# Optimization experiments

Hardware: AMD Instinct MI355X
Metric: run time of the kernel (lower is better)

Reference implementation:

```python
import jax, jax.numpy as jnp
import numpy as np
import math

PAD_IDX = 1
BOS_IDX = 2
B, S, T = 32, 128, 64
E, H, L, V = 256, 512, 2, 32000


def _lstm_cell(gates, c):
    # torch gate order: i, f, g, o
    i, f, g, o = jnp.split(gates, 4, axis=-1)
    c_new = jax.nn.sigmoid(f) * c + jax.nn.sigmoid(i) * jnp.tanh(g)
    h_new = jax.nn.sigmoid(o) * jnp.tanh(c_new)
    return h_new, c_new


def _run_lstm_layer(x_tbi, Wih, Whh, b, h0, c0):
    def step(carry, x_t):
        h, c = carry
        h2, c2 = _lstm_cell(x_t @ Wih + h @ Whh + b, c)
        return (h2, c2), h2
    (hT, cT), ys = jax.lax.scan(step, (h0, c0), x_tbi)
    return ys, hT, cT


def setup_inputs() -> dict:
    key = jax.random.key(0)
    ks = iter(jax.random.split(key, 40))
    def w(shape, s=0.05):
        return jax.random.normal(next(ks), shape, jnp.float32) * s
    inp = {
        'src_tokens': jax.random.randint(next(ks), (B, S), 0, V, dtype=jnp.int32),
        'tgt_tokens': jax.random.randint(next(ks), (B, T), 0, V, dtype=jnp.int32),
        'src_emb': w((V, E), 0.02),
        'tgt_emb': w((V, E), 0.02),
        'enc_Wih0': w((E, 4 * H)), 'enc_Whh0': w((H, 4 * H)), 'enc_b0': jnp.zeros((4 * H,), jnp.float32),
        'enc_Wih1': w((H, 4 * H)), 'enc_Whh1': w((H, 4 * H)), 'enc_b1': jnp.zeros((4 * H,), jnp.float32),
        'dec_Wih0': w((E + H, 4 * H)), 'dec_Whh0': w((H, 4 * H)), 'dec_b0': jnp.zeros((4 * H,), jnp.float32),
        'dec_Wih1': w((H, 4 * H)), 'dec_Whh1': w((H, 4 * H)), 'dec_b1': jnp.zeros((4 * H,), jnp.float32),
        'attn_W': w((2 * H, H)), 'attn_b': jnp.zeros((H,), jnp.float32),
        'v_w': w((H,)),
        'coal_w': w((L, 1), 0.5), 'coal_b': jnp.zeros((1,), jnp.float32),
        'out_W': w((2 * H + E, V)), 'out_b': jnp.zeros((V,), jnp.float32),
    }
    return inp


def reference(src_tokens, tgt_tokens, src_emb, tgt_emb,
              enc_Wih0, enc_Whh0, enc_b0, enc_Wih1, enc_Whh1, enc_b1,
              dec_Wih0, dec_Whh0, dec_b0, dec_Wih1, dec_Whh1, dec_b1,
              attn_W, attn_b, v_w, coal_w, coal_b, out_W, out_b):
    Bq = src_tokens.shape[0]
    sqrtE_src = np.float32(math.sqrt(src_emb.shape[1]))
    sqrtE_tgt = np.float32(math.sqrt(tgt_emb.shape[1]))

    # ---- Encoder (2-layer LSTM, batch_first; dropout=0 eval) ----
    x = (src_emb[src_tokens] * sqrtE_src).transpose(1, 0, 2)  # (S,B,E)
    z = jnp.zeros((Bq, H), jnp.float32)
    ys0, hA, cA = _run_lstm_layer(x, enc_Wih0, enc_Whh0, enc_b0, z, z)
    ys1, hB, cB = _run_lstm_layer(ys0, enc_Wih1, enc_Whh1, enc_b1, z, z)
    enc_out = ys1.transpose(1, 0, 2)          # (B,S,H)
    hidden = jnp.stack([hA, hB])              # (L,B,H)
    cell = jnp.stack([cA, cB])

    mask = src_tokens != PAD_IDX              # (B,S)
    Wq, We = attn_W[:H], attn_W[H:]
    enc_proj = enc_out @ We                   # (B,S,H) loop-invariant part of attn linear

    def dec_step(carry, tok):
        h, c = carry                          # (L,B,H) each
        emb = jax.nn.relu(tgt_emb[tok] * sqrtE_tgt)          # (B,E)
        # faithful raw reshape (L,B,H) -> (B,H,L), coalesce layers
        q = jax.nn.relu(h.reshape(Bq, H, L) @ coal_w + coal_b)[..., 0]  # (B,H)
        e = jnp.tanh(enc_proj + (q @ Wq + attn_b)[:, None, :])          # (B,S,H)
        score = e @ v_w                                                 # (B,S)
        score = jnp.where(mask, score, np.float32(-1e10))
        a = jax.nn.softmax(score, axis=1)
        wctx = jnp.einsum('bs,bsh->bh', a, enc_out)                     # (B,H)
        xin = jnp.concatenate([emb, wctx], axis=-1)                     # (B,E+H)
        h0n, c0n = _lstm_cell(xin @ dec_Wih0 + h[0] @ dec_Whh0 + dec_b0, c[0])
        h1n, c1n = _lstm_cell(h0n @ dec_Wih1 + h[1] @ dec_Whh1 + dec_b1, c[1])
        logits = jnp.concatenate([h1n, wctx, emb], axis=-1) @ out_W + out_b  # (B,V)
        return (jnp.stack([h0n, h1n]), jnp.stack([c0n, c1n])), logits

    (hF, cF), outs = jax.lax.scan(dec_step, (hidden, cell), tgt_tokens[:, :-1].T)
    first = jnp.full((Bq, 1, out_b.shape[0]), np.float32(BOS_IDX))  # decoder_outputs[:,0]=BOS_IDX
    dec_outputs = jnp.concatenate([first, outs.transpose(1, 0, 2)], axis=1)  # (B,T,V)
    return dec_outputs, hF, cF
```

## Files before the change

### kernel.cpp

```cpp
#include <hip/hip_runtime.h>
#include <hip/hip_bf16.h>

typedef __bf16 bf16x8 __attribute__((ext_vector_type(8)));
typedef float f32x4 __attribute__((ext_vector_type(4)));
typedef unsigned long long u64;

#define DEV static __device__ __forceinline__

constexpr int Bq = 32, Sq = 128, Tq = 64, Eq = 256, Hq = 512, Vq = 32000;
constexpr int G4 = 2048;
constexpr int TD = 63;
constexpr int KOUT = 1280;
constexpr float SQRTE = 16.0f;

DEV float sigf(float x) { return 1.0f / (1.0f + __expf(-x)); }
DEV float tanh_fast(float x) {
    float ax = fabsf(x);
    float t = __expf(-2.f * ax);
    float r = (1.f - t) / (1.f + t);
    return x < 0.f ? -r : r;
}
DEV float tanh_c(float x) {
    float xc = fminf(fmaxf(x, -15.f), 15.f);
    float t = __expf(2.f * xc);
    return (t - 1.f) / (t + 1.f);
}

DEV u64 ldc(const u64* p) {
    return __hip_atomic_load(p, __ATOMIC_RELAXED, __HIP_MEMORY_SCOPE_AGENT);
}
DEV unsigned ldc32(const unsigned* p) {
    return __hip_atomic_load(p, __ATOMIC_RELAXED, __HIP_MEMORY_SCOPE_AGENT);
}
DEV void stc(u64* p, u64 v) {
    __hip_atomic_store(p, v, __ATOMIC_RELAXED, __HIP_MEMORY_SCOPE_AGENT);
}
DEV void stc32(unsigned* p, unsigned v) {
    __hip_atomic_store(p, v, __ATOMIC_RELAXED, __HIP_MEMORY_SCOPE_AGENT);
}
DEV unsigned short bfbits(float f) {
    __bf16 h = (__bf16)f;
    return __builtin_bit_cast(unsigned short, h);
}
DEV float bf2f(unsigned short u) {
    __bf16 h = __builtin_bit_cast(__bf16, u);
    return (float)h;
}
DEV u64 pack4bf(float a, float b, float c, float d) {
    return (u64)bfbits(a) | ((u64)bfbits(b) << 16) |
           ((u64)bfbits(c) << 32) | ((u64)bfbits(d) << 48);
}
DEV u64 pack2f(float a, float b) {
    return (u64)__float_as_uint(a) | ((u64)__float_as_uint(b) << 32);
}

template<bool C> DEV u64 ld64(const u64* p) { return C ? ldc(p) : *p; }
template<bool C> DEV void st64(u64* p, u64 v) { if (C) stc(p, v); else *p = v; }

DEV void gbar(unsigned* flags, int nblk, unsigned epoch) {
    __syncthreads();
    if (threadIdx.x < 64) {
        if (threadIdx.x == 0) {
            asm volatile("s_waitcnt vmcnt(0)" ::: "memory");
            stc32(flags + blockIdx.x * 32, epoch);
        }
        int lane = threadIdx.x;
        for (;;) {
            unsigned v0 = (lane < nblk) ? ldc32(flags + lane * 32) : epoch;
            if (__all((int)(v0 >= epoch))) break;
            __builtin_amdgcn_s_sleep(1);
        }
    }
    __syncthreads();
}

__global__ __launch_bounds__(256) void k_embed_src(const int* __restrict__ tok,
                                                   const float* __restrict__ emb,
                                                   __hip_bfloat16* __restrict__ x)
{
    int idx = blockIdx.x * 256 + threadIdx.x;
    int e = idx & (Eq - 1);
    int r = idx >> 8;
    int b = r & 31, t = r >> 5;
    x[idx] = __float2bfloat16(emb[(size_t)tok[b * Sq + t] * Eq + e] * SQRTE);
}

__global__ __launch_bounds__(256) void k_embed_tgt(const int* __restrict__ tok,
                                                   const float* __restrict__ emb,
                                                   __hip_bfloat16* __restrict__ embt,
                                                   __hip_bfloat16* __restrict__ Xout)
{
    int idx = blockIdx.x * 256 + threadIdx.x;
    int e = idx & (Eq - 1);
    int r = idx >> 8;
    int b = r & 31, t = r >> 5;
    float v = fmaxf(0.f, emb[(size_t)tok[b * Tq + t] * Eq + e] * SQRTE);
    embt[idx] = __float2bfloat16(v);
    Xout[(size_t)r * KOUT + 1024 + e] = __float2bfloat16(v);
}

__global__ __launch_bounds__(256) void k_transpose_bf16(const float* __restrict__ W,
                                                        __hip_bfloat16* __restrict__ Wt,
                                                        int K, int N)
{
    __shared__ float tile[32][33];
    int nb = blockIdx.x * 32, kb = blockIdx.y * 32;
    int c = threadIdx.x & 31, r4 = threadIdx.x >> 5;
    for (int i = 0; i < 32; i += 8)
        tile[r4 + i][c] = W[(size_t)(kb + r4 + i) * N + nb + c];
    __syncthreads();
    for (int i = 0; i < 32; i += 8) {
        int rr = r4 + i;
        Wt[(size_t)(nb + rr) * K + kb + c] = __float2bfloat16(tile[c][rr]);
    }
}

template<bool C>
DEV void stage_a(const u64* src, __bf16* As) {
    int tx = threadIdx.x;
#pragma unroll
    for (int p = 0; p < 8; ++p) {
        int c = tx + p * 256;
        int row = c >> 6, kc = c & 63;
        u64 v0 = ld64<C>(src + c * 2);
        u64 v1 = ld64<C>(src + c * 2 + 1);
        int kd = kc ^ (row & 7);
        *(u64*)(As + row * 512 + kd * 8) = v0;
        *(u64*)(As + row * 512 + kd * 8 + 4) = v1;
    }
}

DEV void mfma_pass(const __bf16* As, const unsigned short* BT, int colB,
                   int kg, int fr, f32x4* acc) {
    const unsigned short* bp = BT + (size_t)colB * 512 + kg * 8;
    int f7 = fr & 7;
#pragma unroll
    for (int k0 = 0; k0 < 512; k0 += 32) {
        int cidx = ((k0 >> 3) | kg) ^ f7;
        bf16x8 bfv = *(const bf16x8*)(bp + k0);
        bf16x8 af0 = *(const bf16x8*)(As + fr * 512 + cidx * 8);
        bf16x8 af1 = *(const bf16x8*)(As + (16 + fr) * 512 + cidx * 8);
        acc[0] = __builtin_amdgcn_mfma_f32_16x16x32_bf16(af0, bfv, acc[0], 0, 0, 0);
        acc[1] = __builtin_amdgcn_mfma_f32_16x16x32_bf16(af1, bfv, acc[1], 0, 0, 0);
    }
}

DEV void mfma_gates(const __bf16* As0, const __bf16* As1,
                    const __hip_bfloat16* B0T, const __hip_bfloat16* B1T,
                    int j0, float* gbuf)
{
    int tx = threadIdx.x, w = tx >> 6, lane = tx & 63;
    int fr = lane & 15, kg = lane >> 4;
    int colB = w * 512 + j0 + fr;
    f32x4 acc[2];
    acc[0] = (f32x4){0.f, 0.f, 0.f, 0.f};
    acc[1] = (f32x4){0.f, 0.f, 0.f, 0.f};
    mfma_pass(As0, (const unsigned short*)B0T, colB, kg, fr, acc);
    if (B1T) mfma_pass(As1, (const unsigned short*)B1T, colB, kg, fr, acc);
    __syncthreads();
    float* gw = gbuf + w * 512;
#pragma unroll
    for (int m = 0; m < 2; ++m)
#pragma unroll
        for (int qd = 0; qd < 4; ++qd)
            gw[(m * 16 + kg * 4 + qd) * 16 + fr] = acc[m][qd];
    __syncthreads();
}

template<bool C>
DEV void cell_epi(const float* gbuf, const float* gadd,
                  const __hip_bfloat16* xpart, const float* bias,
                  float* cbuf, u64* hb, u64* hf,
                  __hip_bfloat16* eb, int ebs, int j0)
{
    int tx = threadIdx.x;
    if (tx >= 128) return;
    int b = tx >> 2, jg = tx & 3;
    int jj0 = jg * 4;
    int j = j0 + jj0;
    float g[4][4];
#pragma unroll
    for (int gi = 0; gi < 4; ++gi) {
        int idx = gi * 512 + b * 16 + jj0;
        float4 gv = *(const float4*)(gbuf + idx);
        g[gi][0] = gv.x; g[gi][1] = gv.y; g[gi][2] = gv.z; g[gi][3] = gv.w;
        if (gadd) {
            float4 ga = *(const float4*)(gadd + idx);
            g[gi][0] += ga.x; g[gi][1] += ga.y; g[gi][2] += ga.z; g[gi][3] += ga.w;
        }
        if (xpart) {
            u64 xv = *(const u64*)((const unsigned short*)xpart + b * 2048 + gi * 512 + j);
#pragma unroll
            for (int e = 0; e < 4; ++e)
                g[gi][e] += bf2f((unsigned short)(xv >> (16 * e)));
        }
        if (bias) {
            float4 bv = *(const float4*)(bias + gi * 512 + j);
            g[gi][0] += bv.x; g[gi][1] += bv.y; g[gi][2] += bv.z; g[gi][3] += bv.w;
        }
    }
    float4 cv = *(float4*)(cbuf + b * 512 + j);
    float cc[4] = {cv.x, cv.y, cv.z, cv.w};
    float hv[4];
#pragma unroll
    for (int e = 0; e < 4; ++e) {
        float cn = sigf(g[1][e]) * cc[e] + sigf(g[0][e]) * tanh_fast(g[2][e]);
        cc[e] = cn;
        hv[e] = sigf(g[3][e]) * tanh_fast(cn);
    }
    *(float4*)(cbuf + b * 512 + j) = make_float4(cc[0], cc[1], cc[2], cc[3]);
    u64 hpk = pack4bf(hv[0], hv[1], hv[2], hv[3]);
    st64<C>(hb + ((b * 512 + j) >> 2), hpk);
    st64<C>(hf + ((b * 512 + j) >> 1), pack2f(hv[0], hv[1]));
    st64<C>(hf + ((b * 512 + j) >> 1) + 1, pack2f(hv[2], hv[3]));
    if (eb) st64<C>((u64*)(eb + (size_t)b * ebs + j), hpk);
}

__global__ __launch_bounds__(256) void k_enc_persist(
    const __hip_bfloat16* __restrict__ X0b,
    const __hip_bfloat16* __restrict__ eWhh0T, const __hip_bfloat16* __restrict__ eWih1T,
    const __hip_bfloat16* __restrict__ eWhh1T, const float* __restrict__ eb1,
    __hip_bfloat16* __restrict__ h0b, __hip_bfloat16* __restrict__ h1b,
    float* __restrict__ h0f, float* __restrict__ h1f,
    float* __restrict__ c0, float* __restrict__ c1,
    __hip_bfloat16* __restrict__ ys0b,
    __hip_bfloat16* __restrict__ encb,
    unsigned* __restrict__ flags)
{
    __shared__ __align__(16) char shm[65536];
    __bf16* As0 = (__bf16*)shm;
    __bf16* As1 = (__bf16*)(shm + 32768);
    bool lay1 = blockIdx.x >= 32;
    int j0 = (blockIdx.x & 31) * 16;
    for (int t = 0; t <= 128; ++t) {
        if (!lay1) {
            if (t < 128) {
                stage_a<true>((const u64*)(h0b + (t & 1) * 16384), As0);
                __syncthreads();
                mfma_gates(As0, nullptr, eWhh0T, nullptr, j0, (float*)As0);
                cell_epi<true>((float*)As0, nullptr, X0b + (size_t)t * 32 * 2048, nullptr,
                               c0, (u64*)(h0b + ((t + 1) & 1) * 16384), (u64*)h0f,
                               nullptr, 0, j0);
                if (threadIdx.x < 128) {
                    int b = threadIdx.x >> 2, jg = threadIdx.x & 3;
                    int j = j0 + jg * 4;
                    u64 hpk = ldc((const u64*)(h0b + ((t + 1) & 1) * 16384) + ((b * 512 + j) >> 2));
                    stc((u64*)(ys0b + (size_t)t * 16384 + b * 512 + j), hpk);
                }
            }
        } else {
            if (t >= 1) {
                int s = t - 1;
                stage_a<true>((const u64*)(ys0b + (size_t)s * 16384), As0);
                stage_a<true>((const u64*)(h1b + (s & 1) * 16384), As1);
                __syncthreads();
                mfma_gates(As0, As1, eWih1T, eWhh1T, j0, (float*)As0);
                cell_epi<true>((float*)As0, nullptr, nullptr, eb1,
                               c1, (u64*)(h1b + ((s + 1) & 1) * 16384), (u64*)h1f,
                               encb + s * 512, 128 * 512, j0);
            }
        }
        gbar(flags, 64, (unsigned)(t + 1));
    }
}

__global__ __launch_bounds__(256) void k_dattn(
    const __hip_bfloat16* __restrict__ enc_projb, const __hip_bfloat16* __restrict__ enc_outb,
    const int* __restrict__ src_tok, const float* __restrict__ v_w,
    const float* __restrict__ attn_W, const float* __restrict__ attn_b,
    const float* __restrict__ coal_w, const float* __restrict__ coal_b,
    const __hip_bfloat16* __restrict__ dWhh0T, const __hip_bfloat16* __restrict__ dWhh1T,
    const float* __restrict__ h0fc, const float* __restrict__ h1fc,
    const __hip_bfloat16* __restrict__ h0bc, const __hip_bfloat16* __restrict__ h1bc,
    __hip_bfloat16* __restrict__ wctxb, __hip_bfloat16* __restrict__ XoutT,
    float* __restrict__ g0slab, float* __restrict__ g1slab)
{
    __shared__ __align__(16) char shm[32768];
    __shared__ float rinvs;
    __bf16* As0 = (__bf16*)shm;
    int bid = blockIdx.x, tx = threadIdx.x;

    if (bid < 32) {
        int b = bid;
        float* q   = (float*)shm;
        float* aqs = q + 512;
        float* vws = aqs + 512;
        float* ws  = vws + 512;
        const float* hrow = (b < 16) ? (h0fc + b * 1024) : (h1fc + (b - 16) * 1024);
        float cw0 = coal_w[0], cw1 = coal_w[1], cb = coal_b[0];
        for (int j = tx; j < 512; j += 256) {
            float2 pv = *(const float2*)(hrow + 2 * j);
            q[j] = fmaxf(0.f, pv.x * cw0 + pv.y * cw1 + cb);
        }
        for (int i = tx; i < 512; i += 256) vws[i] = v_w[i];
        __syncthreads();
        float a0 = attn_b[tx], a1 = attn_b[tx + 256];
#pragma unroll 8
        for (int j = 0; j < 512; ++j) {
            float qj = q[j];
            a0 += qj * attn_W[(size_t)j * 512 + tx];
            a1 += qj * attn_W[(size_t)j * 512 + tx + 256];
        }
        aqs[tx] = a0; aqs[tx + 256] = a1;
        __syncthreads();
        int s = tx >> 1, half = tx & 1;
        const unsigned short* epr = (const unsigned short*)enc_projb
                                    + ((size_t)(b * 128 + s)) * 512 + half * 256;
        float s0 = 0.f, s1 = 0.f, s2 = 0.f, s3 = 0.f;
#pragma unroll 4
        for (int ii = 0; ii < 256; ii += 8) {
            bf16x8 f8 = *(const bf16x8*)(epr + ii);
            int ib = half * 256 + ii;
            s0 += tanh_c((float)f8[0] + aqs[ib])     * vws[ib];
            s1 += tanh_c((float)f8[1] + aqs[ib + 1]) * vws[ib + 1];
            s2 += tanh_c((float)f8[2] + aqs[ib + 2]) * vws[ib + 2];
            s3 += tanh_c((float)f8[3] + aqs[ib + 3]) * vws[ib + 3];
            s0 += tanh_c((float)f8[4] + aqs[ib + 4]) * vws[ib + 4];
            s1 += tanh_c((float)f8[5] + aqs[ib + 5]) * vws[ib + 5];
            s2 += tanh_c((float)f8[6] + aqs[ib + 6]) * vws[ib + 6];
            s3 += tanh_c((float)f8[7] + aqs[ib + 7]) * vws[ib + 7];
        }
        float p = (s0 + s1) + (s2 + s3);
        p += __shfl_xor(p, 1, 64);
        if (half == 0)
            ws[s] = (src_tok[b * 128 + s] != 1) ? __expf(p) : 0.f;
        __syncthreads();
        if (tx < 64) {
            float ss = ws[tx] + ws[tx + 64];
#pragma unroll
            for (int o = 32; o > 0; o >>= 1) ss += __shfl_down(ss, o, 64);
            if (tx == 0) rinvs = 1.0f / ss;
        }
        __syncthreads();
        float rinv = rinvs;
        const unsigned short* eo = (const unsigned short*)enc_outb + (size_t)b * 65536;
        int i0 = tx * 2;
        float c0a = 0.f, c1a = 0.f;
#pragma unroll 4
        for (int s2i = 0; s2i < 128; ++s2i) {
            unsigned pk2 = *(const unsigned*)(eo + (size_t)s2i * 512 + i0);
            float wv = ws[s2i];
            c0a += wv * bf2f((unsigned short)(pk2 & 0xffffu));
            c1a += wv * bf2f((unsigned short)(pk2 >> 16));
        }
        c0a *= rinv; c1a *= rinv;
        unsigned pk = (unsigned)bfbits(c0a) | ((unsigned)bfbits(c1a) << 16);
        *((unsigned*)wctxb + ((b * 512 + i0) >> 1)) = pk;
        *((unsigned*)XoutT + (((size_t)b * KOUT + 512 + i0) >> 1)) = pk;
    } else {
        int tile = (bid < 64) ? bid - 32 : bid - 64;
        const __hip_bfloat16* hsrc = (bid < 64) ? h0bc : h1bc;
        const __hip_bfloat16* WT = (bid < 64) ? dWhh0T : dWhh1T;
        float* slab = ((bid < 64) ? g0slab : g1slab) + tile * 2048;
        int j0 = tile * 16;
        stage_a<false>((const u64*)hsrc, As0);
        __syncthreads();
        int w = tx >> 6, lane = tx & 63;
        int fr = lane & 15, kg = lane >> 4;
        int colB = w * 512 + j0 + fr;
        f32x4 acc[2];
        acc[0] = (f32x4){0.f, 0.f, 0.f, 0.f};
        acc[1] = (f32x4){0.f, 0.f, 0.f, 0.f};
        mfma_pass(As0, (const unsigned short*)WT, colB, kg, fr, acc);
        float* outp = slab + w * 512;
#pragma unroll
        for (int m = 0; m < 2; ++m)
#pragma unroll
            for (int qd = 0; qd < 4; ++qd)
                outp[(m * 16 + kg * 4 + qd) * 16 + fr] = acc[m][qd];
    }
}

__global__ __launch_bounds__(256) void k_dcell0(
    const __hip_bfloat16* __restrict__ wctxb, const __hip_bfloat16* __restrict__ Wih0wT,
    const __hip_bfloat16* __restrict__ xpart, const float* __restrict__ g0slab,
    float* __restrict__ c0d, __hip_bfloat16* __restrict__ hb_nxt, float* __restrict__ hf_nxt)
{
    __shared__ __align__(16) char shm[32768];
    __bf16* As0 = (__bf16*)shm;
    int j0 = blockIdx.x * 16;
    stage_a<false>((const u64*)wctxb, As0);
    __syncthreads();
    mfma_gates(As0, nullptr, Wih0wT, nullptr, j0, (float*)As0);
    cell_epi<false>((float*)As0, g0slab + blockIdx.x * 2048, xpart, nullptr,
                    c0d, (u64*)hb_nxt, (u64*)hf_nxt, nullptr, 0, j0);
}

__global__ __launch_bounds__(256) void k_dcell1(
    const __hip_bfloat16* __restrict__ h0b_nxt, const __hip_bfloat16* __restrict__ Wih1T,
    const float* __restrict__ db1, const float* __restrict__ g1slab,
    float* __restrict__ c1d, __hip_bfloat16* __restrict__ hb_nxt, float* __restrict__ hf_nxt,
    __hip_bfloat16* __restrict__ XoutT)
{
    __shared__ __align__(16) char shm[32768];
    __bf16* As0 = (__bf16*)shm;
    int j0 = blockIdx.x * 16;
    stage_a<false>((const u64*)h0b_nxt, As0);
    __syncthreads();
    mfma_gates(As0, nullptr, Wih1T, nullptr, j0, (float*)As0);
    cell_epi<false>((float*)As0, g1slab + blockIdx.x * 2048, nullptr, db1,
                    c1d, (u64*)hb_nxt, (u64*)hf_nxt, XoutT, KOUT, j0);
}

__global__ __launch_bounds__(256) void k_mfma(
    const __hip_bfloat16* __restrict__ A, const __hip_bfloat16* __restrict__ BT,
    const float* __restrict__ bias, float* __restrict__ Cf,
    __hip_bfloat16* __restrict__ Cb, int M, int N, int K)
{
    __shared__ __bf16 As[128][72];
    __shared__ __bf16 Bs[128][72];
    const unsigned short* Aw = (const unsigned short*)A;
    const unsigned short* Bw = (const unsigned short*)BT;
    int n0 = blockIdx.x * 128, m0 = blockIdx.y * 128;
    int tx = threadIdx.x;
    int w = tx >> 6, lane = tx & 63;
    int wm = (w >> 1) * 64, wn = (w & 1) * 64;
    int fr = lane & 15, kg = lane >> 4;
    f32x4 acc[4][4];
#pragma unroll
    for (int mi = 0; mi < 4; mi++)
#pragma unroll
        for (int ni = 0; ni < 4; ni++) acc[mi][ni] = (f32x4){0.f, 0.f, 0.f, 0.f};

    for (int k0 = 0; k0 < K; k0 += 64) {
        __syncthreads();
#pragma unroll
        for (int p = 0; p < 4; p++) {
            int ch = tx + p * 256;
            int r = ch >> 3, cc = (ch & 7) * 8;
            uint4 va = {0u, 0u, 0u, 0u};
            int m = m0 + r;
            if (m < M) va = *(const uint4*)(Aw + (size_t)m * K + k0 + cc);
            *(uint4*)(&As[r][cc]) = va;
            uint4 vb = *(const uint4*)(Bw + (size_t)(n0 + r) * K + k0 + cc);
            *(uint4*)(&Bs[r][cc]) = vb;
        }
        __syncthreads();
#pragma unroll
        for (int kk = 0; kk < 64; kk += 32) {
            bf16x8 af[4], bfv[4];
#pragma unroll
            for (int i = 0; i < 4; i++) {
                af[i]  = *(const bf16x8*)(&As[wm + i * 16 + fr][kk + kg * 8]);
                bfv[i] = *(const bf16x8*)(&Bs[wn + i * 16 + fr][kk + kg * 8]);
            }
#pragma unroll
            for (int mi = 0; mi < 4; mi++)
#pragma unroll
                for (int ni = 0; ni < 4; ni++)
                    acc[mi][ni] = __builtin_amdgcn_mfma_f32_16x16x32_bf16(
                        af[mi], bfv[ni], acc[mi][ni], 0, 0, 0);
        }
    }
#pragma unroll
    for (int ni = 0; ni < 4; ni++) {
        int n = n0 + wn + ni * 16 + fr;
        float bv = bias ? bias[n] : 0.f;
#pragma unroll
        for (int mi = 0; mi < 4; mi++) {
#pragma unroll
            for (int qd = 0; qd < 4; qd++) {
                int R = m0 + wm + mi * 16 + kg * 4 + qd;
                if (R < M) {
                    float v = acc[mi][ni][qd] + bv;
                    if (Cf) Cf[(size_t)R * N + n] = v;
                    else    Cb[(size_t)R * N + n] = __float2bfloat16(v);
                }
            }
        }
    }
}

__global__ __launch_bounds__(256) void k_init_dec(
    const float* __restrict__ h0e, const float* __restrict__ h1e,
    const float* __restrict__ c0e, const float* __restrict__ c1e,
    float* __restrict__ h0fd, float* __restrict__ h1fd,
    __hip_bfloat16* __restrict__ h0bd, __hip_bfloat16* __restrict__ h1bd,
    float* __restrict__ c0d, float* __restrict__ c1d)
{
    int idx = blockIdx.x * 256 + threadIdx.x;
    float a = h0e[idx], b = h1e[idx];
    h0fd[idx] = a; h1fd[idx] = b;
    h0bd[idx] = __float2bfloat16(a);
    h1bd[idx] = __float2bfloat16(b);
    c0d[idx] = c0e[idx];
    c1d[idx] = c1e[idx];
}

__global__ __launch_bounds__(256) void k_bos(float* __restrict__ out)
{
    int b = blockIdx.y;
    int i = blockIdx.x * 256 + threadIdx.x;
    out[(size_t)b * (Tq * Vq) + i] = 2.0f;
}

__global__ __launch_bounds__(256) void k_finalize(
    const float* __restrict__ h0f, const float* __restrict__ h1f,
    const float* __restrict__ c0f, const float* __restrict__ c1f,
    float* __restrict__ out)
{
    int idx = blockIdx.x * 256 + threadIdx.x;
    size_t base = (size_t)Bq * Tq * Vq;
    out[base + idx] = h0f[idx];
    out[base + 16384 + idx] = h1f[idx];
    out[base + 32768 + idx] = c0f[idx];
    out[base + 49152 + idx] = c1f[idx];
}

__global__ __launch_bounds__(256) void k_logits(
    const __hip_bfloat16* __restrict__ A, const __hip_bfloat16* __restrict__ Bt,
    const float* __restrict__ bias, float* __restrict__ out)
{
    __shared__ __bf16 As[128][72];
    __shared__ __bf16 Bs[128][72];
    const unsigned short* Aw = (const unsigned short*)A;
    const unsigned short* Bw = (const unsigned short*)Bt;
    int n0 = blockIdx.x * 128, m0 = blockIdx.y * 128;
    int tx = threadIdx.x;
    int w = tx >> 6, lane = tx & 63;
    int wm = (w >> 1) * 64, wn = (w & 1) * 64;
    int fr = lane & 15, kg = lane >> 4;
    f32x4 acc[4][4];
#pragma unroll
    for (int mi = 0; mi < 4; mi++)
#pragma unroll
        for (int ni = 0; ni < 4; ni++) acc[mi][ni] = (f32x4){0.f, 0.f, 0.f, 0.f};

    for (int k0 = 0; k0 < 1280; k0 += 64) {
        __syncthreads();
#pragma unroll
        for (int p = 0; p < 4; p++) {
            int ch = tx + p * 256;
            int r = ch >> 3, cc = (ch & 7) * 8;
            uint4 va = {0u, 0u, 0u, 0u};
            int m = m0 + r;
            if (m < 2016) va = *(const uint4*)(Aw + (size_t)m * 1280 + k0 + cc);
            *(uint4*)(&As[r][cc]) = va;
            uint4 vb = *(const uint4*)(Bw + (size_t)(n0 + r) * 1280 + k0 + cc);
            *(uint4*)(&Bs[r][cc]) = vb;
        }
        __syncthreads();
#pragma unroll
        for (int kk = 0; kk < 64; kk += 32) {
            bf16x8 af[4], bfv[4];
#pragma unroll
            for (int i = 0; i < 4; i++) {
                af[i]  = *(const bf16x8*)(&As[wm + i * 16 + fr][kk + kg * 8]);
                bfv[i] = *(const bf16x8*)(&Bs[wn + i * 16 + fr][kk + kg * 8]);
            }
#pragma unroll
            for (int mi = 0; mi < 4; mi++)
#pragma unroll
                for (int ni = 0; ni < 4; ni++)
                    acc[mi][ni] = __builtin_amdgcn_mfma_f32_16x16x32_bf16(
                        af[mi], bfv[ni], acc[mi][ni], 0, 0, 0);
        }
    }
#pragma unroll
    for (int ni = 0; ni < 4; ni++) {
        int n = n0 + wn + ni * 16 + fr;
        float bv = bias[n];
#pragma unroll
        for (int mi = 0; mi < 4; mi++) {
#pragma unroll
            for (int qd = 0; qd < 4; qd++) {
                int R = m0 + wm + mi * 16 + kg * 4 + qd;
                if (R < 2016) {
                    int bb = R & 31, ts = R >> 5;
                    out[(size_t)bb * (Tq * Vq) + (size_t)(ts + 1) * Vq + n] =
                        acc[mi][ni][qd] + bv;
                }
            }
        }
    }
}

extern "C" void kernel_launch(void* const* d_in, const int* in_sizes, int n_in,
                              void* d_out, int out_size, void* d_ws, size_t ws_size,
                              hipStream_t stream)
{
    (void)in_sizes; (void)n_in; (void)out_size; (void)ws_size;
    const int*   src_tok = (const int*)  d_in[0];
    const int*   tgt_tok = (const int*)  d_in[1];
    const float* src_emb = (const float*)d_in[2];
    const float* tgt_emb = (const float*)d_in[3];
    const float* eWih0   = (const float*)d_in[4];
    const float* eWhh0   = (const float*)d_in[5];
    const float* eb0     = (const float*)d_in[6];
    const float* eWih1   = (const float*)d_in[7];
    const float* eWhh1   = (const float*)d_in[8];
    const float* eb1     = (const float*)d_in[9];
    const float* dWih0   = (const float*)d_in[10];
    const float* dWhh0   = (const float*)d_in[11];
    const float* db0     = (const float*)d_in[12];
    const float* dWih1   = (const float*)d_in[13];
    const float* dWhh1   = (const float*)d_in[14];
    const float* db1     = (const float*)d_in[15];
    const float* attn_W  = (const float*)d_in[16];
    const float* attn_b  = (const float*)d_in[17];
    const float* v_w     = (const float*)d_in[18];
    const float* coal_w  = (const float*)d_in[19];
    const float* coal_b  = (const float*)d_in[20];
    const float* out_W   = (const float*)d_in[21];
    const float* out_b   = (const float*)d_in[22];
    float* out = (float*)d_out;

    char* ws = (char*)d_ws;
    size_t off = 0;
    auto alloc = [&](size_t bytes) -> char* {
        char* p = ws + off;
        off += (bytes + 255) & ~(size_t)255;
        return p;
    };
    typedef __hip_bfloat16 BF;
    BF* X0b     = (BF*)alloc(4096ull * 2048 * 2);
    BF* Xembb   = (BF*)alloc(2016ull * 2048 * 2);
    BF* x_srcb  = (BF*)alloc(4096ull * 256 * 2);
    BF* embtb   = (BF*)alloc(2016ull * 256 * 2);
    BF* ys0b    = (BF*)alloc(128ull * 16384 * 2);
    BF* enc_outb  = (BF*)alloc(4096ull * 512 * 2);
    BF* enc_projb = (BF*)alloc(4096ull * 512 * 2);
    BF* wctxb     = (BF*)alloc(16384ull * 2);
    BF* Xout      = (BF*)alloc(2016ull * 1280 * 2);
    BF* Wt        = (BF*)alloc(32000ull * 1280 * 2);
    BF* eWhh0T  = (BF*)alloc(2048ull * 512 * 2);
    BF* eWih1T  = (BF*)alloc(2048ull * 512 * 2);
    BF* eWhh1T  = (BF*)alloc(2048ull * 512 * 2);
    BF* dWih0wT = (BF*)alloc(2048ull * 512 * 2);
    BF* dWhh0T  = (BF*)alloc(2048ull * 512 * 2);
    BF* dWih1T  = (BF*)alloc(2048ull * 512 * 2);
    BF* dWhh1T  = (BF*)alloc(2048ull * 512 * 2);
    BF* eWih0T  = (BF*)alloc(2048ull * 256 * 2);
    BF* dWih0eT = (BF*)alloc(2048ull * 256 * 2);
    BF* WeT     = (BF*)alloc(512ull * 512 * 2);
    BF* h0b_e   = (BF*)alloc(2ull * 16384 * 2);
    BF* h1b_e   = (BF*)alloc(2ull * 16384 * 2);
    float* h0f_e = (float*)alloc(16384ull * 4);
    float* h1f_e = (float*)alloc(16384ull * 4);
    float* c0e   = (float*)alloc(16384ull * 4);
    float* c1e   = (float*)alloc(16384ull * 4);
    float* h0fd  = (float*)alloc(2ull * 16384 * 4);
    float* h1fd  = (float*)alloc(2ull * 16384 * 4);
    BF* h0bd     = (BF*)alloc(2ull * 16384 * 2);
    BF* h1bd     = (BF*)alloc(2ull * 16384 * 2);
    float* c0d   = (float*)alloc(16384ull * 4);
    float* c1d   = (float*)alloc(16384ull * 4);
    float* g0slab = (float*)alloc(32ull * 2048 * 4);
    float* g1slab = (float*)alloc(32ull * 2048 * 4);
    unsigned* encFlags = (unsigned*)alloc(64 * 32 * 4);

    hipMemsetAsync(encFlags, 0, 64 * 32 * 4, stream);
    hipMemsetAsync(h0b_e, 0, 2 * 16384 * 2, stream);
    hipMemsetAsync(h1b_e, 0, 2 * 16384 * 2, stream);
    hipMemsetAsync(c0e, 0, 16384 * 4, stream);
    hipMemsetAsync(c1e, 0, 16384 * 4, stream);

    k_embed_src<<<4096, 256, 0, stream>>>(src_tok, src_emb, x_srcb);
    k_embed_tgt<<<2016, 256, 0, stream>>>(tgt_tok, tgt_emb, embtb, Xout);

    k_transpose_bf16<<<dim3(64, 16), 256, 0, stream>>>(eWhh0, eWhh0T, 512, 2048);
    k_transpose_bf16<<<dim3(64, 16), 256, 0, stream>>>(eWih1, eWih1T, 512, 2048);
    k_transpose_bf16<<<dim3(64, 16), 256, 0, stream>>>(eWhh1, eWhh1T, 512, 2048);
    k_transpose_bf16<<<dim3(64, 16), 256, 0, stream>>>(dWih0 + 256 * 2048, dWih0wT, 512, 2048);
    k_transpose_bf16<<<dim3(64, 16), 256, 0, stream>>>(dWhh0, dWhh0T, 512, 2048);
    k_transpose_bf16<<<dim3(64, 16), 256, 0, stream>>>(dWih1, dWih1T, 512, 2048);
    k_transpose_bf16<<<dim3(64, 16), 256, 0, stream>>>(dWhh1, dWhh1T, 512, 2048);
    k_transpose_bf16<<<dim3(64, 8), 256, 0, stream>>>(eWih0, eWih0T, 256, 2048);
    k_transpose_bf16<<<dim3(64, 8), 256, 0, stream>>>(dWih0, dWih0eT, 256, 2048);
    k_transpose_bf16<<<dim3(16, 16), 256, 0, stream>>>(attn_W + 512 * 512, WeT, 512, 512);
    k_transpose_bf16<<<dim3(1000, 40), 256, 0, stream>>>(out_W, Wt, 1280, 32000);

    k_mfma<<<dim3(16, 32), 256, 0, stream>>>(x_srcb, eWih0T, eb0, nullptr, X0b, 4096, 2048, 256);
    k_mfma<<<dim3(16, 16), 256, 0, stream>>>(embtb, dWih0eT, db0, nullptr, Xembb, 2016, 2048, 256);
    k_bos<<<dim3(125, 32), 256, 0, stream>>>(out);

    k_enc_persist<<<64, 256, 0, stream>>>(X0b, eWhh0T, eWih1T, eWhh1T, eb1,
                                          h0b_e, h1b_e, h0f_e, h1f_e, c0e, c1e,
                                          ys0b, enc_outb, encFlags);

    k_mfma<<<dim3(4, 32), 256, 0, stream>>>(enc_outb, WeT, nullptr, nullptr, enc_projb, 4096, 512, 512);

    k_init_dec<<<64, 256, 0, stream>>>(h0f_e, h1f_e, c0e, c1e,
                                       h0fd, h1fd, h0bd, h1bd, c0d, c1d);

    for (int t = 0; t < TD; ++t) {
        int cur = t & 1, nxt = cur ^ 1;
        BF* XoutT = Xout + (size_t)t * 32 * KOUT;
        k_dattn<<<96, 256, 0, stream>>>(enc_projb, enc_outb, src_tok, v_w,
                                        attn_W, attn_b, coal_w, coal_b,
                                        dWhh0T, dWhh1T,
                                        h0fd + cur * 16384, h1fd + cur * 16384,
                                        h0bd + cur * 16384, h1bd + cur * 16384,
                                        wctxb, XoutT, g0slab, g1slab);
        k_dcell0<<<32, 256, 0, stream>>>(wctxb, dWih0wT,
                                         Xembb + (size_t)t * 32 * 2048, g0slab,
                                         c0d, h0bd + nxt * 16384, h0fd + nxt * 16384);
        k_dcell1<<<32, 256, 0, stream>>>(h0bd + nxt * 16384, dWih1T, db1, g1slab,
                                         c1d, h1bd + nxt * 16384, h1fd + nxt * 16384,
                                         XoutT);
    }

    k_finalize<<<64, 256, 0, stream>>>(h0fd + (TD & 1) * 16384, h1fd + (TD & 1) * 16384,
                                       c0d, c1d, out);
    k_logits<<<dim3(250, 16), 256, 0, stream>>>(Xout, Wt, out_b, out);
}
```

Measured before the change: 5.480 ms.

## Replace encoder global barrier with flag dataflow waits and fuse decoder recurrent GEMMs

The persistent encoder kernel drops the all-block barrier per step. Each layer's blocks now wait only on the per-block progress flags they depend on, so layer 0 can run ahead of layer 1 in a wavefront pipeline. The decoder no longer computes the Whh products inside the attention kernel through global slabs; each cell kernel does both input and hidden GEMMs from shared memory. Ten weight transposes are also batched into one launch. The risk is weaker overlap in the decoder, since the attention kernel now uses 32 blocks and the hidden GEMMs move onto the serial cell path.

```diff
diff --git a/kernel.cpp b/kernel.cpp
--- a/kernel.cpp
+++ b/kernel.cpp
@@ -8,7 +8,6 @@
 #define DEV static __device__ __forceinline__
 
 constexpr int Bq = 32, Sq = 128, Tq = 64, Eq = 256, Hq = 512, Vq = 32000;
-constexpr int G4 = 2048;
 constexpr int TD = 63;
 constexpr int KOUT = 1280;
 constexpr float SQRTE = 16.0f;
@@ -53,21 +52,18 @@
 DEV u64 pack2f(float a, float b) {
     return (u64)__float_as_uint(a) | ((u64)__float_as_uint(b) << 32);
 }
-
-template<bool C> DEV u64 ld64(const u64* p) { return C ? ldc(p) : *p; }
-template<bool C> DEV void st64(u64* p, u64 v) { if (C) stc(p, v); else *p = v; }
-
-DEV void gbar(unsigned* flags, int nblk, unsigned epoch) {
+template<bool C> DEV u64 ld64g(const u64* p) { return C ? ldc(p) : *p; }
+template<bool C> DEV void st64g(u64* p, u64 v) { if (C) stc(p, v); else *p = v; }
+DEV void drain_vm() { asm volatile("s_waitcnt vmcnt(0)" ::: "memory"); }
+
+DEV void encwait(unsigned* flags, unsigned need0, unsigned need1) {
     __syncthreads();
     if (threadIdx.x < 64) {
-        if (threadIdx.x == 0) {
-            asm volatile("s_waitcnt vmcnt(0)" ::: "memory");
-            stc32(flags + blockIdx.x * 32, epoch);
-        }
         int lane = threadIdx.x;
+        unsigned need = (lane < 32) ? need0 : need1;
         for (;;) {
-            unsigned v0 = (lane < nblk) ? ldc32(flags + lane * 32) : epoch;
-            if (__all((int)(v0 >= epoch))) break;
+            unsigned v = ldc32(flags + lane * 32);
+            if (__all((int)(v >= need))) break;
             __builtin_amdgcn_s_sleep(1);
         }
     }
@@ -115,6 +111,33 @@
     }
 }
 
+struct TD10 {
+    const float* s[10];
+    __hip_bfloat16* d[10];
+    int K[10];
+    int N[10];
+};
+__global__ __launch_bounds__(256) void k_transpose_multi(TD10 td)
+{
+    __shared__ float tile[32][33];
+    int m = blockIdx.y;
+    int K = td.K[m], N = td.N[m];
+    int ntn = N >> 5;
+    int nb = (blockIdx.x % ntn) * 32;
+    int kb = (blockIdx.x / ntn) * 32;
+    if (kb >= K) return;
+    const float* W = td.s[m];
+    __hip_bfloat16* Wt = td.d[m];
+    int c = threadIdx.x & 31, r4 = threadIdx.x >> 5;
+    for (int i = 0; i < 32; i += 8)
+        tile[r4 + i][c] = W[(size_t)(kb + r4 + i) * N + nb + c];
+    __syncthreads();
+    for (int i = 0; i < 32; i += 8) {
+        int rr = r4 + i;
+        Wt[(size_t)(nb + rr) * K + kb + c] = __float2bfloat16(tile[c][rr]);
+    }
+}
+
 template<bool C>
 DEV void stage_a(const u64* src, __bf16* As) {
     int tx = threadIdx.x;
@@ -122,8 +145,8 @@
     for (int p = 0; p < 8; ++p) {
         int c = tx + p * 256;
         int row = c >> 6, kc = c & 63;
-        u64 v0 = ld64<C>(src + c * 2);
-        u64 v1 = ld64<C>(src + c * 2 + 1);
+        u64 v0 = ld64g<C>(src + c * 2);
+        u64 v1 = ld64g<C>(src + c * 2 + 1);
         int kd = kc ^ (row & 7);
         *(u64*)(As + row * 512 + kd * 8) = v0;
         *(u64*)(As + row * 512 + kd * 8 + 4) = v1;
@@ -168,7 +191,7 @@
 }
 
 template<bool C>
-DEV void cell_epi(const float* gbuf, const float* gadd,
+DEV void cell_epi(const float* gbuf,
                   const __hip_bfloat16* xpart, const float* bias,
                   float* cbuf, u64* hb, u64* hf,
                   __hip_bfloat16* eb, int ebs, int j0)
@@ -184,10 +207,6 @@
         int idx = gi * 512 + b * 16 + jj0;
         float4 gv = *(const float4*)(gbuf + idx);
         g[gi][0] = gv.x; g[gi][1] = gv.y; g[gi][2] = gv.z; g[gi][3] = gv.w;
-        if (gadd) {
-            float4 ga = *(const float4*)(gadd + idx);
-            g[gi][0] += ga.x; g[gi][1] += ga.y; g[gi][2] += ga.z; g[gi][3] += ga.w;
-        }
         if (xpart) {
             u64 xv = *(const u64*)((const unsigned short*)xpart + b * 2048 + gi * 512 + j);
 #pragma unroll
@@ -210,10 +229,10 @@
     }
     *(float4*)(cbuf + b * 512 + j) = make_float4(cc[0], cc[1], cc[2], cc[3]);
     u64 hpk = pack4bf(hv[0], hv[1], hv[2], hv[3]);
-    st64<C>(hb + ((b * 512 + j) >> 2), hpk);
-    st64<C>(hf + ((b * 512 + j) >> 1), pack2f(hv[0], hv[1]));
-    st64<C>(hf + ((b * 512 + j) >> 1) + 1, pack2f(hv[2], hv[3]));
-    if (eb) st64<C>((u64*)(eb + (size_t)b * ebs + j), hpk);
+    st64g<C>(hb + ((b * 512 + j) >> 2), hpk);
+    st64g<C>(hf + ((b * 512 + j) >> 1), pack2f(hv[0], hv[1]));
+    st64g<C>(hf + ((b * 512 + j) >> 1) + 1, pack2f(hv[2], hv[3]));
+    if (eb) st64g<C>((u64*)(eb + (size_t)b * ebs + j), hpk);
 }
 
 __global__ __launch_bounds__(256) void k_enc_persist(
@@ -232,174 +251,135 @@
     __bf16* As1 = (__bf16*)(shm + 32768);
     bool lay1 = blockIdx.x >= 32;
     int j0 = (blockIdx.x & 31) * 16;
-    for (int t = 0; t <= 128; ++t) {
-        if (!lay1) {
-            if (t < 128) {
-                stage_a<true>((const u64*)(h0b + (t & 1) * 16384), As0);
-                __syncthreads();
-                mfma_gates(As0, nullptr, eWhh0T, nullptr, j0, (float*)As0);
-                cell_epi<true>((float*)As0, nullptr, X0b + (size_t)t * 32 * 2048, nullptr,
-                               c0, (u64*)(h0b + ((t + 1) & 1) * 16384), (u64*)h0f,
-                               nullptr, 0, j0);
-                if (threadIdx.x < 128) {
-                    int b = threadIdx.x >> 2, jg = threadIdx.x & 3;
-                    int j = j0 + jg * 4;
-                    u64 hpk = ldc((const u64*)(h0b + ((t + 1) & 1) * 16384) + ((b * 512 + j) >> 2));
-                    stc((u64*)(ys0b + (size_t)t * 16384 + b * 512 + j), hpk);
-                }
+
+    if (!lay1) {
+        for (int t = 0; t < 128; ++t) {
+            encwait(flags, (unsigned)t, 0u);
+            stage_a<true>((const u64*)(h0b + (t & 1) * 16384), As0);
+            __syncthreads();
+            mfma_gates(As0, nullptr, eWhh0T, nullptr, j0, (float*)As0);
+            cell_epi<true>((float*)As0, X0b + (size_t)t * 32 * 2048, nullptr,
+                           c0, (u64*)(h0b + ((t + 1) & 1) * 16384), (u64*)h0f,
+                           ys0b + (size_t)t * 16384, 512, j0);
+            __syncthreads();
+            if (threadIdx.x == 0) {
+                drain_vm();
+                stc32(flags + blockIdx.x * 32, (unsigned)(t + 1));
             }
-        } else {
-            if (t >= 1) {
-                int s = t - 1;
-                stage_a<true>((const u64*)(ys0b + (size_t)s * 16384), As0);
-                stage_a<true>((const u64*)(h1b + (s & 1) * 16384), As1);
-                __syncthreads();
-                mfma_gates(As0, As1, eWih1T, eWhh1T, j0, (float*)As0);
-                cell_epi<true>((float*)As0, nullptr, nullptr, eb1,
-                               c1, (u64*)(h1b + ((s + 1) & 1) * 16384), (u64*)h1f,
-                               encb + s * 512, 128 * 512, j0);
+        }
+    } else {
+        for (int s = 0; s < 128; ++s) {
+            encwait(flags, (unsigned)(s + 1), (unsigned)s);
+            stage_a<true>((const u64*)(ys0b + (size_t)s * 16384), As0);
+            stage_a<true>((const u64*)(h1b + (s & 1) * 16384), As1);
+            __syncthreads();
+            mfma_gates(As0, As1, eWih1T, eWhh1T, j0, (float*)As0);
+            cell_epi<true>((float*)As0, nullptr, eb1,
+                           c1, (u64*)(h1b + ((s + 1) & 1) * 16384), (u64*)h1f,
+                           encb + s * 512, 128 * 512, j0);
+            __syncthreads();
+            if (threadIdx.x == 0) {
+                drain_vm();
+                stc32(flags + blockIdx.x * 32, (unsigned)(s + 1));
             }
         }
-        gbar(flags, 64, (unsigned)(t + 1));
-    }
-}
-
-__global__ __launch_bounds__(256) void k_dattn(
+    }
+}
+
+__global__ __launch_bounds__(256) void k_dattn2(
     const __hip_bfloat16* __restrict__ enc_projb, const __hip_bfloat16* __restrict__ enc_outb,
     const int* __restrict__ src_tok, const float* __restrict__ v_w,
     const float* __restrict__ attn_W, const float* __restrict__ attn_b,
     const float* __restrict__ coal_w, const float* __restrict__ coal_b,
-    const __hip_bfloat16* __restrict__ dWhh0T, const __hip_bfloat16* __restrict__ dWhh1T,
     const float* __restrict__ h0fc, const float* __restrict__ h1fc,
-    const __hip_bfloat16* __restrict__ h0bc, const __hip_bfloat16* __restrict__ h1bc,
-    __hip_bfloat16* __restrict__ wctxb, __hip_bfloat16* __restrict__ XoutT,
-    float* __restrict__ g0slab, float* __restrict__ g1slab)
-{
-    __shared__ __align__(16) char shm[32768];
+    __hip_bfloat16* __restrict__ wctxb, __hip_bfloat16* __restrict__ XoutT)
+{
+    __shared__ float q[512];
+    __shared__ float aqs[512];
+    __shared__ float vws[512];
+    __shared__ float ws[128];
     __shared__ float rinvs;
+    int b = blockIdx.x, tx = threadIdx.x;
+
+    const float* hrow = (b < 16) ? (h0fc + b * 1024) : (h1fc + (b - 16) * 1024);
+    float cw0 = coal_w[0], cw1 = coal_w[1], cb = coal_b[0];
+    for (int j = tx; j < 512; j += 256) {
+        float2 pv = *(const float2*)(hrow + 2 * j);
+        q[j] = fmaxf(0.f, pv.x * cw0 + pv.y * cw1 + cb);
+    }
+    for (int i = tx; i < 512; i += 256) vws[i] = v_w[i];
+    __syncthreads();
+    float a0 = attn_b[tx], a1 = attn_b[tx + 256];
+#pragma unroll 8
+    for (int j = 0; j < 512; ++j) {
+        float qj = q[j];
+        a0 += qj * attn_W[(size_t)j * 512 + tx];
+        a1 += qj * attn_W[(size_t)j * 512 + tx + 256];
+    }
+    aqs[tx] = a0; aqs[tx + 256] = a1;
+    __syncthreads();
+    int s = tx >> 1, half = tx & 1;
+    const unsigned short* epr = (const unsigned short*)enc_projb
+                                + ((size_t)(b * 128 + s)) * 512 + half * 256;
+    float s0 = 0.f, s1 = 0.f, s2 = 0.f, s3 = 0.f;
+#pragma unroll 4
+    for (int ii = 0; ii < 256; ii += 8) {
+        bf16x8 f8 = *(const bf16x8*)(epr + ii);
+        int ib = half * 256 + ii;
+        s0 += tanh_c((float)f8[0] + aqs[ib])     * vws[ib];
+        s1 += tanh_c((float)f8[1] + aqs[ib + 1]) * vws[ib + 1];
+        s2 += tanh_c((float)f8[2] + aqs[ib + 2]) * vws[ib + 2];
+        s3 += tanh_c((float)f8[3] + aqs[ib + 3]) * vws[ib + 3];
+        s0 += tanh_c((float)f8[4] + aqs[ib + 4]) * vws[ib + 4];
+        s1 += tanh_c((float)f8[5] + aqs[ib + 5]) * vws[ib + 5];
+        s2 += tanh_c((float)f8[6] + aqs[ib + 6]) * vws[ib + 6];
+        s3 += tanh_c((float)f8[7] + aqs[ib + 7]) * vws[ib + 7];
+    }
+    float p = (s0 + s1) + (s2 + s3);
+    p += __shfl_xor(p, 1, 64);
+    if (half == 0)
+        ws[s] = (src_tok[b * 128 + s] != 1) ? __expf(p) : 0.f;
+    __syncthreads();
+    if (tx < 64) {
+        float ss = ws[tx] + ws[tx + 64];
+#pragma unroll
+        for (int o = 32; o > 0; o >>= 1) ss += __shfl_down(ss, o, 64);
+        if (tx == 0) rinvs = 1.0f / ss;
+    }
+    __syncthreads();
+    float rinv = rinvs;
+    const unsigned short* eo = (const unsigned short*)enc_outb + (size_t)b * 65536;
+    int i0 = tx * 2;
+    float c0a = 0.f, c1a = 0.f;
+#pragma unroll 4
+    for (int s2i = 0; s2i < 128; ++s2i) {
+        unsigned pk2 = *(const unsigned*)(eo + (size_t)s2i * 512 + i0);
+        float wv = ws[s2i];
+        c0a += wv * bf2f((unsigned short)(pk2 & 0xffffu));
+        c1a += wv * bf2f((unsigned short)(pk2 >> 16));
+    }
+    c0a *= rinv; c1a *= rinv;
+    unsigned pk = (unsigned)bfbits(c0a) | ((unsigned)bfbits(c1a) << 16);
+    *((unsigned*)wctxb + ((b * 512 + i0) >> 1)) = pk;
+    *((unsigned*)XoutT + (((size_t)b * KOUT + 512 + i0) >> 1)) = pk;
+}
+
+__global__ __launch_bounds__(256) void k_rec(
+    const __hip_bfloat16* __restrict__ A0, const __hip_bfloat16* __restrict__ B0T,
+    const __hip_bfloat16* __restrict__ A1, const __hip_bfloat16* __restrict__ B1T,
+    const __hip_bfloat16* __restrict__ xpart, const float* __restrict__ bias,
+    float* __restrict__ cbuf, float* __restrict__ hf, __hip_bfloat16* __restrict__ hb,
+    __hip_bfloat16* __restrict__ ebf16, int ebs)
+{
+    __shared__ __align__(16) char shm[65536];
     __bf16* As0 = (__bf16*)shm;
-    int bid = blockIdx.x, tx = threadIdx.x;
-
-    if (bid < 32) {
-        int b = bid;
-        float* q   = (float*)shm;
-        float* aqs = q + 512;
-        float* vws = aqs + 512;
-        float* ws  = vws + 512;
-        const float* hrow = (b < 16) ? (h0fc + b * 1024) : (h1fc + (b - 16) * 1024);
-        float cw0 = coal_w[0], cw1 = coal_w[1], cb = coal_b[0];
-        for (int j = tx; j < 512; j += 256) {
-            float2 pv = *(const float2*)(hrow + 2 * j);
-            q[j] = fmaxf(0.f, pv.x * cw0 + pv.y * cw1 + cb);
-        }
-        for (int i = tx; i < 512; i += 256) vws[i] = v_w[i];
-        __syncthreads();
-        float a0 = attn_b[tx], a1 = attn_b[tx + 256];
-#pragma unroll 8
-        for (int j = 0; j < 512; ++j) {
-            float qj = q[j];
-            a0 += qj * attn_W[(size_t)j * 512 + tx];
-            a1 += qj * attn_W[(size_t)j * 512 + tx + 256];
-        }
-        aqs[tx] = a0; aqs[tx + 256] = a1;
-        __syncthreads();
-        int s = tx >> 1, half = tx & 1;
-        const unsigned short* epr = (const unsigned short*)enc_projb
-                                    + ((size_t)(b * 128 + s)) * 512 + half * 256;
-        float s0 = 0.f, s1 = 0.f, s2 = 0.f, s3 = 0.f;
-#pragma unroll 4
-        for (int ii = 0; ii < 256; ii += 8) {
-            bf16x8 f8 = *(const bf16x8*)(epr + ii);
-            int ib = half * 256 + ii;
-            s0 += tanh_c((float)f8[0] + aqs[ib])     * vws[ib];
-            s1 += tanh_c((float)f8[1] + aqs[ib + 1]) * vws[ib + 1];
-            s2 += tanh_c((float)f8[2] + aqs[ib + 2]) * vws[ib + 2];
-            s3 += tanh_c((float)f8[3] + aqs[ib + 3]) * vws[ib + 3];
-            s0 += tanh_c((float)f8[4] + aqs[ib + 4]) * vws[ib + 4];
-            s1 += tanh_c((float)f8[5] + aqs[ib + 5]) * vws[ib + 5];
-            s2 += tanh_c((float)f8[6] + aqs[ib + 6]) * vws[ib + 6];
-            s3 += tanh_c((float)f8[7] + aqs[ib + 7]) * vws[ib + 7];
-        }
-        float p = (s0 + s1) + (s2 + s3);
-        p += __shfl_xor(p, 1, 64);
-        if (half == 0)
-            ws[s] = (src_tok[b * 128 + s] != 1) ? __expf(p) : 0.f;
-        __syncthreads();
-        if (tx < 64) {
-            float ss = ws[tx] + ws[tx + 64];
-#pragma unroll
-            for (int o = 32; o > 0; o >>= 1) ss += __shfl_down(ss, o, 64);
-            if (tx == 0) rinvs = 1.0f / ss;
-        }
-        __syncthreads();
-        float rinv = rinvs;
-        const unsigned short* eo = (const unsigned short*)enc_outb + (size_t)b * 65536;
-        int i0 = tx * 2;
-        float c0a = 0.f, c1a = 0.f;
-#pragma unroll 4
-        for (int s2i = 0; s2i < 128; ++s2i) {
-            unsigned pk2 = *(const unsigned*)(eo + (size_t)s2i * 512 + i0);
-            float wv = ws[s2i];
-            c0a += wv * bf2f((unsigned short)(pk2 & 0xffffu));
-            c1a += wv * bf2f((unsigned short)(pk2 >> 16));
-        }
-        c0a *= rinv; c1a *= rinv;
-        unsigned pk = (unsigned)bfbits(c0a) | ((unsigned)bfbits(c1a) << 16);
-        *((unsigned*)wctxb + ((b * 512 + i0) >> 1)) = pk;
-        *((unsigned*)XoutT + (((size_t)b * KOUT + 512 + i0) >> 1)) = pk;
-    } else {
-        int tile = (bid < 64) ? bid - 32 : bid - 64;
-        const __hip_bfloat16* hsrc = (bid < 64) ? h0bc : h1bc;
-        const __hip_bfloat16* WT = (bid < 64) ? dWhh0T : dWhh1T;
-        float* slab = ((bid < 64) ? g0slab : g1slab) + tile * 2048;
-        int j0 = tile * 16;
-        stage_a<false>((const u64*)hsrc, As0);
-        __syncthreads();
-        int w = tx >> 6, lane = tx & 63;
-        int fr = lane & 15, kg = lane >> 4;
-        int colB = w * 512 + j0 + fr;
-        f32x4 acc[2];
-        acc[0] = (f32x4){0.f, 0.f, 0.f, 0.f};
-        acc[1] = (f32x4){0.f, 0.f, 0.f, 0.f};
-        mfma_pass(As0, (const unsigned short*)WT, colB, kg, fr, acc);
-        float* outp = slab + w * 512;
-#pragma unroll
-        for (int m = 0; m < 2; ++m)
-#pragma unroll
-            for (int qd = 0; qd < 4; ++qd)
-                outp[(m * 16 + kg * 4 + qd) * 16 + fr] = acc[m][qd];
-    }
-}
-
-__global__ __launch_bounds__(256) void k_dcell0(
-    const __hip_bfloat16* __restrict__ wctxb, const __hip_bfloat16* __restrict__ Wih0wT,
-    const __hip_bfloat16* __restrict__ xpart, const float* __restrict__ g0slab,
-    float* __restrict__ c0d, __hip_bfloat16* __restrict__ hb_nxt, float* __restrict__ hf_nxt)
-{
-    __shared__ __align__(16) char shm[32768];
-    __bf16* As0 = (__bf16*)shm;
+    __bf16* As1 = (__bf16*)(shm + 32768);
     int j0 = blockIdx.x * 16;
-    stage_a<false>((const u64*)wctxb, As0);
-    __syncthreads();
-    mfma_gates(As0, nullptr, Wih0wT, nullptr, j0, (float*)As0);
-    cell_epi<false>((float*)As0, g0slab + blockIdx.x * 2048, xpart, nullptr,
-                    c0d, (u64*)hb_nxt, (u64*)hf_nxt, nullptr, 0, j0);
-}
-
-__global__ __launch_bounds__(256) void k_dcell1(
-    const __hip_bfloat16* __restrict__ h0b_nxt, const __hip_bfloat16* __restrict__ Wih1T,
-    const float* __restrict__ db1, const float* __restrict__ g1slab,
-    float* __restrict__ c1d, __hip_bfloat16* __restrict__ hb_nxt, float* __restrict__ hf_nxt,
-    __hip_bfloat16* __restrict__ XoutT)
-{
-    __shared__ __align__(16) char shm[32768];
-    __bf16* As0 = (__bf16*)shm;
-    int j0 = blockIdx.x * 16;
-    stage_a<false>((const u64*)h0b_nxt, As0);
-    __syncthreads();
-    mfma_gates(As0, nullptr, Wih1T, nullptr, j0, (float*)As0);
-    cell_epi<false>((float*)As0, g1slab + blockIdx.x * 2048, nullptr, db1,
-                    c1d, (u64*)hb_nxt, (u64*)hf_nxt, XoutT, KOUT, j0);
+    stage_a<false>((const u64*)A0, As0);
+    stage_a<false>((const u64*)A1, As1);
+    __syncthreads();
+    mfma_gates(As0, As1, B0T, B1T, j0, (float*)As0);
+    cell_epi<false>((float*)As0, xpart, bias, cbuf, (u64*)hb, (u64*)hf, ebf16, ebs, j0);
 }
 
 __global__ __launch_bounds__(256) void k_mfma(
@@ -645,8 +625,6 @@
     BF* h1bd     = (BF*)alloc(2ull * 16384 * 2);
     float* c0d   = (float*)alloc(16384ull * 4);
     float* c1d   = (float*)alloc(16384ull * 4);
-    float* g0slab = (float*)alloc(32ull * 2048 * 4);
-    float* g1slab = (float*)alloc(32ull * 2048 * 4);
     unsigned* encFlags = (unsigned*)alloc(64 * 32 * 4);
 
     hipMemsetAsync(encFlags, 0, 64 * 32 * 4, stream);
@@ -658,16 +636,18 @@
     k_embed_src<<<4096, 256, 0, stream>>>(src_tok, src_emb, x_srcb);
     k_embed_tgt<<<2016, 256, 0, stream>>>(tgt_tok, tgt_emb, embtb, Xout);
 
-    k_transpose_bf16<<<dim3(64, 16), 256, 0, stream>>>(eWhh0, eWhh0T, 512, 2048);
-    k_transpose_bf16<<<dim3(64, 16), 256, 0, stream>>>(eWih1, eWih1T, 512, 2048);
-    k_transpose_bf16<<<dim3(64, 16), 256, 0, stream>>>(eWhh1, eWhh1T, 512, 2048);
-    k_transpose_bf16<<<dim3(64, 16), 256, 0, stream>>>(dWih0 + 256 * 2048, dWih0wT, 512, 2048);
-    k_transpose_bf16<<<dim3(64, 16), 256, 0, stream>>>(dWhh0, dWhh0T, 512, 2048);
-    k_transpose_bf16<<<dim3(64, 16), 256, 0, stream>>>(dWih1, dWih1T, 512, 2048);
-    k_transpose_bf16<<<dim3(64, 16), 256, 0, stream>>>(dWhh1, dWhh1T, 512, 2048);
-    k_transpose_bf16<<<dim3(64, 8), 256, 0, stream>>>(eWih0, eWih0T, 256, 2048);
-    k_transpose_bf16<<<dim3(64, 8), 256, 0, stream>>>(dWih0, dWih0eT, 256, 2048);
-    k_transpose_bf16<<<dim3(16, 16), 256, 0, stream>>>(attn_W + 512 * 512, WeT, 512, 512);
+    TD10 td;
+    td.s[0] = eWhh0;              td.d[0] = eWhh0T;  td.K[0] = 512; td.N[0] = 2048;
+    td.s[1] = eWih1;              td.d[1] = eWih1T;  td.K[1] = 512; td.N[1] = 2048;
+    td.s[2] = eWhh1;              td.d[2] = eWhh1T;  td.K[2] = 512; td.N[2] = 2048;
+    td.s[3] = dWih0 + 256 * 2048; td.d[3] = dWih0wT; td.K[3] = 512; td.N[3] = 2048;
+    td.s[4] = dWhh0;              td.d[4] = dWhh0T;  td.K[4] = 512; td.N[4] = 2048;
+    td.s[5] = dWih1;              td.d[5] = dWih1T;  td.K[5] = 512; td.N[5] = 2048;
+    td.s[6] = dWhh1;              td.d[6] = dWhh1T;  td.K[6] = 512; td.N[6] = 2048;
+    td.s[7] = eWih0;              td.d[7] = eWih0T;  td.K[7] = 256; td.N[7] = 2048;
+    td.s[8] = dWih0;              td.d[8] = dWih0eT; td.K[8] = 256; td.N[8] = 2048;
+    td.s[9] = attn_W + 512 * 512; td.d[9] = WeT;     td.K[9] = 512; td.N[9] = 512;
+    k_transpose_multi<<<dim3(1024, 10), 256, 0, stream>>>(td);
     k_transpose_bf16<<<dim3(1000, 40), 256, 0, stream>>>(out_W, Wt, 1280, 32000);
 
     k_mfma<<<dim3(16, 32), 256, 0, stream>>>(x_srcb, eWih0T, eb0, nullptr, X0b, 4096, 2048, 256);
@@ -686,18 +666,20 @@
     for (int t = 0; t < TD; ++t) {
         int cur = t & 1, nxt = cur ^ 1;
         BF* XoutT = Xout + (size_t)t * 32 * KOUT;
-        k_dattn<<<96, 256, 0, stream>>>(enc_projb, enc_outb, src_tok, v_w,
-                                        attn_W, attn_b, coal_w, coal_b,
-                                        dWhh0T, dWhh1T,
-                                        h0fd + cur * 16384, h1fd + cur * 16384,
-                                        h0bd + cur * 16384, h1bd + cur * 16384,
-                                        wctxb, XoutT, g0slab, g1slab);
-        k_dcell0<<<32, 256, 0, stream>>>(wctxb, dWih0wT,
-                                         Xembb + (size_t)t * 32 * 2048, g0slab,
-                                         c0d, h0bd + nxt * 16384, h0fd + nxt * 16384);
-        k_dcell1<<<32, 256, 0, stream>>>(h0bd + nxt * 16384, dWih1T, db1, g1slab,
-                                         c1d, h1bd + nxt * 16384, h1fd + nxt * 16384,
-                                         XoutT);
+        k_dattn2<<<32, 256, 0, stream>>>(enc_projb, enc_outb, src_tok, v_w,
+                                         attn_W, attn_b, coal_w, coal_b,
+                                         h0fd + cur * 16384, h1fd + cur * 16384,
+                                         wctxb, XoutT);
+        k_rec<<<32, 256, 0, stream>>>(wctxb, dWih0wT,
+                                      h0bd + cur * 16384, dWhh0T,
+                                      Xembb + (size_t)t * 32 * 2048, nullptr,
+                                      c0d, h0fd + nxt * 16384, h0bd + nxt * 16384,
+                                      nullptr, 0);
+        k_rec<<<32, 256, 0, stream>>>(h0bd + nxt * 16384, dWih1T,
+                                      h1bd + cur * 16384, dWhh1T,
+                                      nullptr, db1,
+                                      c1d, h1fd + nxt * 16384, h1bd + nxt * 16384,
+                                      XoutT, KOUT);
     }
 
     k_finalize<<<64, 256, 0, stream>>>(h0fd + (TD & 1) * 16384, h1fd + (TD & 1) * 16384,
```

New measurement: 5.297 ms. 1.03x faster.
